# Performance work log

Hardware: AMD Instinct MI355X
Metric: run time of the kernel (lower is better)

The kernel has to match this reference:

```python
import jax, jax.numpy as jnp
import numpy as np

N_EMBD = 448
HEAD_SIZE = 64

def setup_inputs() -> dict:
    key = jax.random.key(0)
    k1, k2, k3, k4 = jax.random.split(key, 4)
    B, T = 16, 2048
    x = jax.random.normal(k1, (B, T, N_EMBD), dtype=jnp.float32)
    # nn.Linear(n_embd, head_size, bias=False): weight shape (head_size, n_embd); y = x @ W.T
    s = 1.0 / np.sqrt(N_EMBD)
    Wk = jax.random.uniform(k2, (HEAD_SIZE, N_EMBD), jnp.float32, -s, s)
    Wq = jax.random.uniform(k3, (HEAD_SIZE, N_EMBD), jnp.float32, -s, s)
    Wv = jax.random.uniform(k4, (HEAD_SIZE, N_EMBD), jnp.float32, -s, s)
    return {"x": x, "Wk": Wk, "Wq": Wq, "Wv": Wv}

def reference(x, Wk, Wq, Wv):
    B, T, C = x.shape
    k = jnp.einsum('btc,hc->bth', x, Wk)  # (B,T,H)
    q = jnp.einsum('btc,hc->bth', x, Wq)
    v = jnp.einsum('btc,hc->bth', x, Wv)
    scale = 1.0 / jnp.sqrt(jnp.float32(C))  # NOTE: scales by sqrt(n_embd), as in source
    wei = jnp.einsum('bth,bsh->bts', q, k) * scale  # (B,T,T)
    causal = jnp.tril(jnp.ones((T, T), dtype=bool))
    wei = jnp.where(causal[None, :, :], wei, -jnp.inf)
    wei = jax.nn.softmax(wei, axis=-1)
    # dropout is identity in eval mode
    out = jnp.einsum('bts,bsh->bth', wei, v)  # (B,T,H)
    return out
```

## Files before the change

### kernel.cpp

```cpp
#include <hip/hip_runtime.h>
#include <math.h>

#define BT 32768
#define NC 448
#define NH 64
#define TT 2048

typedef __bf16 bf16x8 __attribute__((ext_vector_type(8)));
typedef float  f32x4  __attribute__((ext_vector_type(4)));

__device__ __forceinline__ unsigned short f2bf(float f) {
  unsigned u = __builtin_bit_cast(unsigned, f);
  return (unsigned short)((u + 0x7FFFu + ((u >> 16) & 1u)) >> 16);
}
__device__ __forceinline__ ushort4 f2bf4(float4 v) {
  ushort4 b; b.x = f2bf(v.x); b.y = f2bf(v.y); b.z = f2bf(v.z); b.w = f2bf(v.w);
  return b;
}


__global__ __launch_bounds__(256) void proj_kernel(
    const float* __restrict__ x, const float* __restrict__ Wk,
    const float* __restrict__ Wq, const float* __restrict__ Wv,
    unsigned short* __restrict__ kws, unsigned short* __restrict__ qws,
    unsigned short* __restrict__ vws)
{
  __shared__ unsigned short xs[2][4096];
  __shared__ unsigned short wsm[2][4096];
  const int tid = threadIdx.x;
  const int w = tid >> 6, lane = tid & 63;
  const int q = lane >> 4, l15 = lane & 15;
  const int r0 = blockIdx.x * 64;
  const int p = blockIdx.y;
  const float* W = (p == 0) ? Wk : ((p == 1) ? Wq : Wv);

  f32x4 acc[4];
#pragma unroll
  for (int i = 0; i < 4; ++i) acc[i] = f32x4{0.f, 0.f, 0.f, 0.f};

  const int c0 = (tid & 15) * 4, r_ = tid >> 4;

  float4 xr[4], wr[4];
#pragma unroll
  for (int i = 0; i < 4; ++i) {
    xr[i] = *(const float4*)&x[(size_t)(r0 + r_ + 16 * i) * NC + c0];
    wr[i] = *(const float4*)&W[(size_t)(r_ + 16 * i) * NC + c0];
  }

  for (int ch = 0; ch < 7; ++ch) {
    const int cur = ch & 1;
#pragma unroll
    for (int i = 0; i < 4; ++i) {
      int r = r_ + 16 * i;
      int off = r * 64 + (((c0 >> 3) ^ (r & 7)) << 3) + (c0 & 7);
      *(ushort4*)&xs[cur][off]  = f2bf4(xr[i]);
      *(ushort4*)&wsm[cur][off] = f2bf4(wr[i]);
    }
    __syncthreads();
    if (ch < 6) {
      int kc = (ch + 1) * 64;
#pragma unroll
      for (int i = 0; i < 4; ++i) {
        xr[i] = *(const float4*)&x[(size_t)(r0 + r_ + 16 * i) * NC + kc + c0];
        wr[i] = *(const float4*)&W[(size_t)(r_ + 16 * i) * NC + kc + c0];
      }
    }
#pragma unroll
    for (int ks = 0; ks < 2; ++ks) {
      int xrow = w * 16 + l15;
      int g = q + 4 * ks;
      bf16x8 xf = *(const bf16x8*)&xs[cur][xrow * 64 + ((g ^ (xrow & 7)) << 3)];
#pragma unroll
      for (int t = 0; t < 4; ++t) {
        int wrow = t * 16 + l15;
        bf16x8 wf = *(const bf16x8*)&wsm[cur][wrow * 64 + ((g ^ (wrow & 7)) << 3)];
        if (p == 0)
          acc[t] = __builtin_amdgcn_mfma_f32_16x16x32_bf16(wf, xf, acc[t], 0, 0, 0);
        else
          acc[t] = __builtin_amdgcn_mfma_f32_16x16x32_bf16(xf, wf, acc[t], 0, 0, 0);
      }
    }
  }

  const size_t tile = (size_t)blockIdx.x * 4096;
  if (p == 0) {
#pragma unroll
    for (int t = 0; t < 4; ++t) {
      int j = w * 16 + l15;
      ushort4 bb; bb.x = f2bf(acc[t][0]); bb.y = f2bf(acc[t][1]);
      bb.z = f2bf(acc[t][2]); bb.w = f2bf(acc[t][3]);
      *(ushort4*)&kws[tile + j * 64 + (((2 * t + (q >> 1)) ^ (j & 7)) << 3) + ((q & 1) << 2)] = bb;
    }
  } else if (p == 1) {
    const float qs = 0.068161075f;
#pragma unroll
    for (int t = 0; t < 4; ++t) {
      int h = t * 16 + l15;
#pragma unroll
      for (int rr = 0; rr < 4; ++rr) {
        int R = r0 + w * 16 + q * 4 + rr;
        qws[(size_t)R * 64 + h] = f2bf(acc[t][rr] * qs);
      }
    }
  } else {
#pragma unroll
    for (int t = 0; t < 4; ++t) {
      int h = t * 16 + l15;
      ushort4 bb; bb.x = f2bf(acc[t][0]); bb.y = f2bf(acc[t][1]);
      bb.z = f2bf(acc[t][2]); bb.w = f2bf(acc[t][3]);
      *(ushort4*)&vws[tile + h * 64 + (((2 * w + (q >> 1)) ^ (h & 7)) << 3) + ((q & 1) << 2)] = bb;
    }
  }
}

__global__ __launch_bounds__(256) void attn_partial(
    const unsigned short* __restrict__ kws, const unsigned short* __restrict__ qws,
    const unsigned short* __restrict__ vws, float* __restrict__ out,
    float* __restrict__ opart, float* __restrict__ mlpart)
{
  __shared__ unsigned short ksm[2][4096];
  __shared__ unsigned short vtm[2][4096];
  __shared__ unsigned short psm[4096];
  const int bx = blockIdx.x, b = blockIdx.y;
  int qt, kt0, ktn, ci; bool direct;
  if (bx < 16)      { qt = 16 + bx; kt0 = 0;  ktn = 16;     ci = 0; direct = false; }
  else if (bx < 32) { qt = 47 - bx; kt0 = 16; ktn = qt + 1; ci = 1; direct = false; }
  else              { qt = 47 - bx; kt0 = 0;  ktn = qt + 1; ci = 0; direct = true;  }
  const int nt = ktn - kt0;

  const int tid = threadIdx.x;
  const int w = tid >> 6, lane = tid & 63;
  const int q = lane >> 4, l15 = lane & 15;
  const int t0 = b * TT + qt * 64;
  const int l7 = l15 & 7;

  bf16x8 qf[2];
#pragma unroll
  for (int ks = 0; ks < 2; ++ks)
    qf[ks] = *(const bf16x8*)&qws[(size_t)(t0 + w * 16 + l15) * 64 + 32 * ks + q * 8];

  f32x4 oacc[4];
#pragma unroll
  for (int ht = 0; ht < 4; ++ht) oacc[ht] = f32x4{0.f, 0.f, 0.f, 0.f};
  float m_i = -INFINITY, l_i = 0.f;

  uint4 kr0, kr1, vr0, vr1;
  {
    const unsigned short* kt_ = kws + (size_t)(b * 32 + kt0) * 4096;
    const unsigned short* vt_ = vws + (size_t)(b * 32 + kt0) * 4096;
    kr0 = *(const uint4*)&kt_[tid * 8];  kr1 = *(const uint4*)&kt_[2048 + tid * 8];
    vr0 = *(const uint4*)&vt_[tid * 8];  vr1 = *(const uint4*)&vt_[2048 + tid * 8];
  }

  for (int it = 0; it < nt; ++it) {
    const int kt = kt0 + it;
    const int cur = it & 1;
    *(uint4*)&ksm[cur][tid * 8] = kr0;  *(uint4*)&ksm[cur][2048 + tid * 8] = kr1;
    *(uint4*)&vtm[cur][tid * 8] = vr0;  *(uint4*)&vtm[cur][2048 + tid * 8] = vr1;
    __syncthreads();
    if (it + 1 < nt) {
      const unsigned short* kt_ = kws + (size_t)(b * 32 + kt + 1) * 4096;
      const unsigned short* vt_ = vws + (size_t)(b * 32 + kt + 1) * 4096;
      kr0 = *(const uint4*)&kt_[tid * 8];  kr1 = *(const uint4*)&kt_[2048 + tid * 8];
      vr0 = *(const uint4*)&vt_[tid * 8];  vr1 = *(const uint4*)&vt_[2048 + tid * 8];
    }

    f32x4 sacc[4];
#pragma unroll
    for (int jt = 0; jt < 4; ++jt) sacc[jt] = f32x4{0.f, 0.f, 0.f, 0.f};
#pragma unroll
    for (int jt = 0; jt < 4; ++jt) {
      int j = jt * 16 + l15;
#pragma unroll
      for (int ks = 0; ks < 2; ++ks) {
        bf16x8 kf = *(const bf16x8*)&ksm[cur][j * 64 + (((q + 4 * ks) ^ (j & 7)) << 3)];
        sacc[jt] = __builtin_amdgcn_mfma_f32_16x16x32_bf16(kf, qf[ks], sacc[jt], 0, 0, 0);
      }
    }

    if (kt == qt) {
      int iloc = w * 16 + l15;
#pragma unroll
      for (int jt = 0; jt < 4; ++jt)
#pragma unroll
        for (int rr = 0; rr < 4; ++rr)
          if (jt * 16 + q * 4 + rr > iloc) sacc[jt][rr] = -INFINITY;
    }

    float mx = -INFINITY;
#pragma unroll
    for (int jt = 0; jt < 4; ++jt)
#pragma unroll
      for (int rr = 0; rr < 4; ++rr) mx = fmaxf(mx, sacc[jt][rr]);
    mx = fmaxf(mx, __shfl_xor(mx, 16));
    mx = fmaxf(mx, __shfl_xor(mx, 32));
    float mn = fmaxf(m_i, mx);
    float alpha = exp2f(m_i - mn);
    m_i = mn;
    float p[4][4], rs = 0.f;
#pragma unroll
    for (int jt = 0; jt < 4; ++jt)
#pragma unroll
      for (int rr = 0; rr < 4; ++rr) {
        float pv = exp2f(sacc[jt][rr] - mn);
        p[jt][rr] = pv; rs += pv;
      }
    rs += __shfl_xor(rs, 16);
    rs += __shfl_xor(rs, 32);
    l_i = l_i * alpha + rs;

    float a_t[4];
#pragma unroll
    for (int rr = 0; rr < 4; ++rr) a_t[rr] = __shfl(alpha, q * 4 + rr);
#pragma unroll
    for (int ht = 0; ht < 4; ++ht)
#pragma unroll
      for (int rr = 0; rr < 4; ++rr) oacc[ht][rr] *= a_t[rr];

    {
      int row = w * 16 + l15;
#pragma unroll
      for (int jt = 0; jt < 4; ++jt) {
        ushort4 bb; bb.x = f2bf(p[jt][0]); bb.y = f2bf(p[jt][1]);
        bb.z = f2bf(p[jt][2]); bb.w = f2bf(p[jt][3]);
        *(ushort4*)&psm[row * 64 + (((2 * jt + (q >> 1)) ^ l7) << 3) + ((q & 1) << 2)] = bb;
      }
    }

#pragma unroll
    for (int ks2 = 0; ks2 < 2; ++ks2) {
      int prow = w * 16 + l15;
      bf16x8 pf = *(const bf16x8*)&psm[prow * 64 + (((q + 4 * ks2) ^ l7) << 3)];
#pragma unroll
      for (int ht = 0; ht < 4; ++ht) {
        int h = ht * 16 + l15;
        bf16x8 vf = *(const bf16x8*)&vtm[cur][h * 64 + (((q + 4 * ks2) ^ l7) << 3)];
        oacc[ht] = __builtin_amdgcn_mfma_f32_16x16x32_bf16(pf, vf, oacc[ht], 0, 0, 0);
      }
    }
  }

  if (direct) {
    float l_t[4];
#pragma unroll
    for (int rr = 0; rr < 4; ++rr) l_t[rr] = __shfl(l_i, q * 4 + rr);
#pragma unroll
    for (int rr = 0; rr < 4; ++rr) {
      float inv = 1.f / l_t[rr];
      int R = t0 + w * 16 + q * 4 + rr;
#pragma unroll
      for (int ht = 0; ht < 4; ++ht)
        out[(size_t)R * 64 + ht * 16 + l15] = oacc[ht][rr] * inv;
    }
  } else {
    const size_t slot = (size_t)(b * 16 + (qt - 16)) * 2 + ci;
    float* Op = opart + slot * 4096;
#pragma unroll
    for (int rr = 0; rr < 4; ++rr) {
      int rloc = w * 16 + q * 4 + rr;
#pragma unroll
      for (int ht = 0; ht < 4; ++ht)
        Op[rloc * 64 + ht * 16 + l15] = oacc[ht][rr];
    }
    if (q == 0) {
      mlpart[slot * 128 + w * 16 + l15]      = m_i;
      mlpart[slot * 128 + 64 + w * 16 + l15] = l_i;
    }
  }
}

__global__ __launch_bounds__(256) void combine_kernel(
    const float* __restrict__ opart, const float* __restrict__ mlpart,
    float* __restrict__ out)
{
  const int qtc = blockIdx.x, b = blockIdx.y;
  const int qt = 16 + qtc;
  const int t = threadIdx.x;
  const int r = t >> 2, c0 = (t & 3) * 16;
  const size_t s0 = (size_t)(b * 16 + qtc) * 2;

  float m0 = mlpart[s0 * 128 + r],       l0 = mlpart[s0 * 128 + 64 + r];
  float m1 = mlpart[(s0 + 1) * 128 + r], l1 = mlpart[(s0 + 1) * 128 + 64 + r];
  float m  = fmaxf(m0, m1);
  float w0 = exp2f(m0 - m), w1 = exp2f(m1 - m);
  float inv = 1.f / (w0 * l0 + w1 * l1);
  w0 *= inv; w1 *= inv;

  const float* O0 = opart + s0 * 4096 + r * 64;
  const float* O1 = opart + (s0 + 1) * 4096 + r * 64;
  float* op = out + (size_t)(b * TT + qt * 64 + r) * 64;
#pragma unroll
  for (int j = 0; j < 4; ++j) {
    float4 a  = *(const float4*)&O0[c0 + j * 4];
    float4 bb = *(const float4*)&O1[c0 + j * 4];
    float4 o;
    o.x = w0 * a.x + w1 * bb.x;  o.y = w0 * a.y + w1 * bb.y;
    o.z = w0 * a.z + w1 * bb.z;  o.w = w0 * a.w + w1 * bb.w;
    *(float4*)&op[c0 + j * 4] = o;
  }
}

extern "C" void kernel_launch(void* const* d_in, const int* in_sizes, int n_in,
                              void* d_out, int out_size, void* d_ws, size_t ws_size,
                              hipStream_t stream) {
  const float* x  = (const float*)d_in[0];
  const float* Wk = (const float*)d_in[1];
  const float* Wq = (const float*)d_in[2];
  const float* Wv = (const float*)d_in[3];
  unsigned short* kws = (unsigned short*)d_ws;
  unsigned short* qws = kws + (size_t)BT * NH;
  unsigned short* vws = qws + (size_t)BT * NH;
  float* opart  = (float*)(vws + (size_t)BT * NH);
  float* mlpart = opart + (size_t)512 * 4096;
  float* out = (float*)d_out;

  proj_kernel<<<dim3(512, 3), 256, 0, stream>>>(x, Wk, Wq, Wv, kws, qws, vws);
  attn_partial<<<dim3(48, 16), 256, 0, stream>>>(kws, qws, vws, out, opart, mlpart);
  combine_kernel<<<dim3(16, 16), 256, 0, stream>>>(opart, mlpart, out);
}
```

Measured before the change: 147.1 us.

## Split KV into 8-tile chunks and fuse combine via last-block atomic reduction

Changes the attention work split so query tiles 8-31 are partitioned into up to four 8-tile KV chunks (80 blocks per batch instead of 48), which balances load across the causal triangle. The separate combine kernel is removed: each partial block publishes its results, increments an atomic counter, and the last block to arrive merges all chunks in-kernel. Counters are zeroed inside the projection kernel. This adds more partial-result traffic and threadfence/atomic overhead in exchange for one fewer launch and better occupancy balance.

Measured after the change: 369.8 us. 2.51x slower.

```diff
diff --git a/kernel.cpp b/kernel.cpp
--- a/kernel.cpp
+++ b/kernel.cpp
@@ -23,7 +23,7 @@
     const float* __restrict__ x, const float* __restrict__ Wk,
     const float* __restrict__ Wq, const float* __restrict__ Wv,
     unsigned short* __restrict__ kws, unsigned short* __restrict__ qws,
-    unsigned short* __restrict__ vws)
+    unsigned short* __restrict__ vws, int* __restrict__ cnt)
 {
   __shared__ unsigned short xs[2][4096];
   __shared__ unsigned short wsm[2][4096];
@@ -34,6 +34,11 @@
   const int p = blockIdx.y;
   const float* W = (p == 0) ? Wk : ((p == 1) ? Wq : Wv);
 
+  if (p == 0 && blockIdx.x < 2) {
+    int idx = blockIdx.x * 256 + tid;
+    if (idx < 384) cnt[idx] = 0;
+  }
+
   f32x4 acc[4];
 #pragma unroll
   for (int i = 0; i < 4; ++i) acc[i] = f32x4{0.f, 0.f, 0.f, 0.f};
@@ -116,16 +121,20 @@
 __global__ __launch_bounds__(256) void attn_partial(
     const unsigned short* __restrict__ kws, const unsigned short* __restrict__ qws,
     const unsigned short* __restrict__ vws, float* __restrict__ out,
-    float* __restrict__ opart, float* __restrict__ mlpart)
+    float* __restrict__ opart, float* __restrict__ mlpart, int* __restrict__ cnt)
 {
   __shared__ unsigned short ksm[2][4096];
   __shared__ unsigned short vtm[2][4096];
   __shared__ unsigned short psm[4096];
+  __shared__ int win;
   const int bx = blockIdx.x, b = blockIdx.y;
-  int qt, kt0, ktn, ci; bool direct;
-  if (bx < 16)      { qt = 16 + bx; kt0 = 0;  ktn = 16;     ci = 0; direct = false; }
-  else if (bx < 32) { qt = 47 - bx; kt0 = 16; ktn = qt + 1; ci = 1; direct = false; }
-  else              { qt = 47 - bx; kt0 = 0;  ktn = qt + 1; ci = 0; direct = true;  }
+  int qt, ci; bool direct;
+  if (bx < 16)      { qt = 8 + (bx >> 1);         ci = bx & 1;        direct = false; }
+  else if (bx < 40) { qt = 16 + (bx - 16) / 3;    ci = (bx - 16) % 3; direct = false; }
+  else if (bx < 72) { qt = 24 + ((bx - 40) >> 2); ci = (bx - 40) & 3; direct = false; }
+  else              { qt = 79 - bx;               ci = 0;             direct = true;  }
+  const int kt0 = direct ? 0 : ci * 8;
+  const int ktn = direct ? (qt + 1) : min(kt0 + 8, qt + 1);
   const int nt = ktn - kt0;
 
   const int tid = threadIdx.x;
@@ -252,9 +261,14 @@
       for (int ht = 0; ht < 4; ++ht)
         out[(size_t)R * 64 + ht * 16 + l15] = oacc[ht][rr] * inv;
     }
-  } else {
-    const size_t slot = (size_t)(b * 16 + (qt - 16)) * 2 + ci;
-    float* Op = opart + slot * 4096;
+    return;
+  }
+
+  const int qi = qt - 8;
+  const int nch = (qt >> 3) + 1;
+  const size_t sbase = (size_t)(b * 24 + qi) * 4;
+  {
+    float* Op = opart + (sbase + ci) * 4096;
 #pragma unroll
     for (int rr = 0; rr < 4; ++rr) {
       int rloc = w * 16 + q * 4 + rr;
@@ -263,40 +277,41 @@
         Op[rloc * 64 + ht * 16 + l15] = oacc[ht][rr];
     }
     if (q == 0) {
-      mlpart[slot * 128 + w * 16 + l15]      = m_i;
-      mlpart[slot * 128 + 64 + w * 16 + l15] = l_i;
-    }
-  }
-}
-
-__global__ __launch_bounds__(256) void combine_kernel(
-    const float* __restrict__ opart, const float* __restrict__ mlpart,
-    float* __restrict__ out)
-{
-  const int qtc = blockIdx.x, b = blockIdx.y;
-  const int qt = 16 + qtc;
-  const int t = threadIdx.x;
-  const int r = t >> 2, c0 = (t & 3) * 16;
-  const size_t s0 = (size_t)(b * 16 + qtc) * 2;
-
-  float m0 = mlpart[s0 * 128 + r],       l0 = mlpart[s0 * 128 + 64 + r];
-  float m1 = mlpart[(s0 + 1) * 128 + r], l1 = mlpart[(s0 + 1) * 128 + 64 + r];
-  float m  = fmaxf(m0, m1);
-  float w0 = exp2f(m0 - m), w1 = exp2f(m1 - m);
-  float inv = 1.f / (w0 * l0 + w1 * l1);
-  w0 *= inv; w1 *= inv;
-
-  const float* O0 = opart + s0 * 4096 + r * 64;
-  const float* O1 = opart + (s0 + 1) * 4096 + r * 64;
-  float* op = out + (size_t)(b * TT + qt * 64 + r) * 64;
+      mlpart[(sbase + ci) * 128 + w * 16 + l15]      = m_i;
+      mlpart[(sbase + ci) * 128 + 64 + w * 16 + l15] = l_i;
+    }
+  }
+  __threadfence();
+  __syncthreads();
+  if (tid == 0) win = (atomicAdd(&cnt[b * 24 + qi], 1) == nch - 1);
+  __syncthreads();
+  if (!win) return;
+
+  __threadfence();
+  const int r = tid >> 2, cc = (tid & 3) * 16;
+  float mc[4], lc[4];
+  float mm = -INFINITY;
+#pragma unroll 4
+  for (int c = 0; c < nch; ++c) {
+    mc[c] = mlpart[(sbase + c) * 128 + r];
+    lc[c] = mlpart[(sbase + c) * 128 + 64 + r];
+    mm = fmaxf(mm, mc[c]);
+  }
+  float denom = 0.f, wgt[4];
+#pragma unroll 4
+  for (int c = 0; c < nch; ++c) { wgt[c] = exp2f(mc[c] - mm); denom += wgt[c] * lc[c]; }
+  const float inv = 1.f / denom;
+  float* op = out + (size_t)(t0 + r) * 64;
 #pragma unroll
   for (int j = 0; j < 4; ++j) {
-    float4 a  = *(const float4*)&O0[c0 + j * 4];
-    float4 bb = *(const float4*)&O1[c0 + j * 4];
-    float4 o;
-    o.x = w0 * a.x + w1 * bb.x;  o.y = w0 * a.y + w1 * bb.y;
-    o.z = w0 * a.z + w1 * bb.z;  o.w = w0 * a.w + w1 * bb.w;
-    *(float4*)&op[c0 + j * 4] = o;
+    float4 acc4 = make_float4(0.f, 0.f, 0.f, 0.f);
+#pragma unroll 4
+    for (int c = 0; c < nch; ++c) {
+      float wc = wgt[c] * inv;
+      float4 a = *(const float4*)&opart[(sbase + c) * 4096 + r * 64 + cc + j * 4];
+      acc4.x += wc * a.x; acc4.y += wc * a.y; acc4.z += wc * a.z; acc4.w += wc * a.w;
+    }
+    *(float4*)&op[cc + j * 4] = acc4;
   }
 }
 
@@ -311,10 +326,10 @@
   unsigned short* qws = kws + (size_t)BT * NH;
   unsigned short* vws = qws + (size_t)BT * NH;
   float* opart  = (float*)(vws + (size_t)BT * NH);
-  float* mlpart = opart + (size_t)512 * 4096;
+  float* mlpart = opart + (size_t)1536 * 4096;
+  int*   cnt    = (int*)(mlpart + (size_t)1536 * 128);
   float* out = (float*)d_out;
 
-  proj_kernel<<<dim3(512, 3), 256, 0, stream>>>(x, Wk, Wq, Wv, kws, qws, vws);
-  attn_partial<<<dim3(48, 16), 256, 0, stream>>>(kws, qws, vws, out, opart, mlpart);
-  combine_kernel<<<dim3(16, 16), 256, 0, stream>>>(opart, mlpart, out);
-}
+  proj_kernel<<<dim3(512, 3), 256, 0, stream>>>(x, Wk, Wq, Wv, kws, qws, vws, cnt);
+  attn_partial<<<dim3(80, 16), 256, 0, stream>>>(kws, qws, vws, out, opart, mlpart, cnt);
+}
```
